# Performance work log

Measured on AMD Instinct MI355X. Metric: run time of the kernel, lower is better.

## Reference

```python
import jax, jax.numpy as jnp
import numpy as np

B, S, E, H = 4, 4096, 256, 2048
EPS = 1e-5

def layernorm(x, g, b):
    mu = jnp.mean(x, axis=-1, keepdims=True)
    var = jnp.mean(jnp.square(x - mu), axis=-1, keepdims=True)
    return (x - mu) * jax.lax.rsqrt(var + EPS) * g + b

def setup_inputs() -> dict:
    key = jax.random.key(0)
    ks = jax.random.split(key, 16)
    sE = 1.0 / np.sqrt(E)
    sH = 1.0 / np.sqrt(H)
    return {
        "x_embeddings": jax.random.normal(ks[0], (B, S, E), dtype=jnp.float32),
        "wq": jax.random.normal(ks[1], (E, E), dtype=jnp.float32) * sE,
        "bq": jnp.zeros((E,), jnp.float32),
        "wk": jax.random.normal(ks[2], (E, E), dtype=jnp.float32) * sE,
        "bk": jnp.zeros((E,), jnp.float32),
        "wv": jax.random.normal(ks[3], (E, E), dtype=jnp.float32) * sE,
        "bv": jnp.zeros((E,), jnp.float32),
        "w0": jax.random.normal(ks[4], (E, E), dtype=jnp.float32) * sE,
        "b0": jnp.zeros((E,), jnp.float32),
        "w1": jax.random.normal(ks[5], (E, H), dtype=jnp.float32) * sE,
        "b1": jnp.zeros((H,), jnp.float32),
        "ln_mlp_g": jnp.ones((H,), jnp.float32),
        "ln_mlp_b": jnp.zeros((H,), jnp.float32),
        "w2": jax.random.normal(ks[6], (H, E), dtype=jnp.float32) * sH,
        "b2": jnp.zeros((E,), jnp.float32),
        "ln1_g": jnp.ones((E,), jnp.float32),
        "ln1_b": jnp.zeros((E,), jnp.float32),
        "ln2_g": jnp.ones((E,), jnp.float32),
        "ln2_b": jnp.zeros((E,), jnp.float32),
    }

def reference(x_embeddings, wq, bq, wk, bk, wv, bv, w0, b0,
              w1, b1, ln_mlp_g, ln_mlp_b, w2, b2,
              ln1_g, ln1_b, ln2_g, ln2_b):
    x = x_embeddings
    q = x @ wq + bq
    k = x @ wk + bk
    v = x @ wv + bv
    # Unscaled, unmasked attention (faithful to source: no 1/sqrt(d), mask unused)
    scores = jnp.einsum('bqd,bkd->bqk', q, k)          # [B,S,S]
    probs = jax.nn.softmax(scores, axis=-1)
    attn = jnp.einsum('bqk,bkd->bqd', probs, v)        # [B,S,E]
    e = layernorm(x + attn, ln1_g, ln1_b) @ w0 + b0
    h = e @ w1 + b1                                     # [B,S,H]
    h = jax.nn.leaky_relu(layernorm(h, ln_mlp_g, ln_mlp_b))  # LnActivation: LN + LeakyReLU
    logits = h @ w2 + b2                                # [B,S,E]
    return layernorm(jax.nn.leaky_relu(logits + e), ln2_g, ln2_b)
```

## Files before the change

kernel.cpp:

```cpp
#include <hip/hip_runtime.h>

typedef unsigned short u16;
typedef unsigned int   u32;
typedef u16   u16x4 __attribute__((ext_vector_type(4)));
typedef u16   u16x8 __attribute__((ext_vector_type(8)));
typedef short s16x8 __attribute__((ext_vector_type(8)));
typedef u32   u32x4 __attribute__((ext_vector_type(4)));
typedef float f32x4 __attribute__((ext_vector_type(4)));
typedef _Float16 f16x8 __attribute__((ext_vector_type(8)));

__device__ __forceinline__ u16 f2b(float f) {
  u32 u = __builtin_bit_cast(u32, f);
  u32 r = (u + 0x7fffu + ((u >> 16) & 1u)) >> 16;
  return (u16)r;
}
__device__ __forceinline__ float b2f(u16 h) {
  return __builtin_bit_cast(float, (u32)h << 16);
}
__device__ __forceinline__ u16 f2h(float f) {
  _Float16 h = (_Float16)f;
  return __builtin_bit_cast(u16, h);
}
__device__ __forceinline__ u32 cvtpk(float a, float b) {
  u32 r; asm("v_cvt_pk_bf16_f32 %0, %1, %2" : "=v"(r) : "v"(a), "v"(b)); return r;
}

__device__ __forceinline__ void async16(void* l, const void* g) {
  __builtin_amdgcn_global_load_lds((const __attribute__((address_space(1))) u32*)g,
                                   (__attribute__((address_space(3))) u32*)l, 16, 0, 0);
}

__device__ __forceinline__ float wave_sum(float v) {
#pragma unroll
  for (int m = 32; m; m >>= 1) v += __shfl_xor(v, m, 64);
  return v;
}

constexpr int BM = 128, BN = 128, BK = 64;

template<bool SPLIT, int OMODE>
__global__ __launch_bounds__(256)
void k_gemm_bt(const u16* __restrict__ Ah, const u16* __restrict__ Al, long lda,
               const u16* __restrict__ Bh, const u16* __restrict__ Bl, long ldb,
               const float* __restrict__ bias,
               float* __restrict__ Cf, u16* __restrict__ Cb, u16* __restrict__ Cl,
               long ldc, int K)
{
  __shared__ u16 lds[(SPLIT ? 4 : 2) * BM * BK];
  const int tid = threadIdx.x;
  const long arow0 = (long)blockIdx.y * BM;
  const long bcol0 = (long)blockIdx.x * BN;

  long offA[4], offB[4];
#pragma unroll
  for (int r = 0; r < 4; ++r) {
    const int off = r * 4096 + tid * 16;
    const int row = off >> 7;
    const int colb = off & 127;
    offA[r] = (arow0 + row) * lda + (colb >> 1);
    offB[r] = (bcol0 + row) * ldb + (colb >> 1);
  }

  const int lane = tid & 63;
  const int wid = tid >> 6;
  const int wr = (wid >> 1) * 64;
  const int wc = (wid & 1) * 64;
  const int fr = lane & 15;
  const int fk = (lane >> 4) * 8;

  f32x4 acc[4][4] = {};

  for (int k0 = 0; k0 < K; k0 += BK) {
#pragma unroll
    for (int r = 0; r < 4; ++r) {
      const int loff = (r * 4096 + tid * 16) >> 1;
      async16(&lds[loff],           Ah + offA[r] + k0);
      async16(&lds[BM*BK + loff],   Bh + offB[r] + k0);
      if constexpr (SPLIT) {
        async16(&lds[2*BM*BK + loff], Al + offA[r] + k0);
        async16(&lds[3*BM*BK + loff], Bl + offB[r] + k0);
      }
    }
    __syncthreads();
#pragma unroll
    for (int kk = 0; kk < BK; kk += 32) {
      s16x8 a[4], b[4];
#pragma unroll
      for (int m = 0; m < 4; ++m)
        a[m] = *(const s16x8*)&lds[(wr + m*16 + fr) * BK + kk + fk];
#pragma unroll
      for (int n = 0; n < 4; ++n)
        b[n] = *(const s16x8*)&lds[BM*BK + (wc + n*16 + fr) * BK + kk + fk];
#pragma unroll
      for (int m = 0; m < 4; ++m)
#pragma unroll
        for (int n = 0; n < 4; ++n)
          acc[m][n] = __builtin_amdgcn_mfma_f32_16x16x32_bf16(a[m], b[n], acc[m][n], 0, 0, 0);
      if constexpr (SPLIT) {
        s16x8 al[4], bl[4];
#pragma unroll
        for (int m = 0; m < 4; ++m)
          al[m] = *(const s16x8*)&lds[2*BM*BK + (wr + m*16 + fr) * BK + kk + fk];
#pragma unroll
        for (int n = 0; n < 4; ++n)
          bl[n] = *(const s16x8*)&lds[3*BM*BK + (wc + n*16 + fr) * BK + kk + fk];
#pragma unroll
        for (int m = 0; m < 4; ++m)
#pragma unroll
          for (int n = 0; n < 4; ++n) {
            acc[m][n] = __builtin_amdgcn_mfma_f32_16x16x32_bf16(a[m], bl[n], acc[m][n], 0, 0, 0);
            acc[m][n] = __builtin_amdgcn_mfma_f32_16x16x32_bf16(al[m], b[n], acc[m][n], 0, 0, 0);
          }
      }
    }
    __syncthreads();
  }

  float bv[4];
#pragma unroll
  for (int n = 0; n < 4; ++n) {
    const long gcol = bcol0 + wc + n*16 + fr;
    bv[n] = bias ? bias[gcol] : 0.f;
  }

#pragma unroll
  for (int m = 0; m < 4; ++m) {
#pragma unroll
    for (int reg = 0; reg < 4; ++reg) {
      const long grow = arow0 + wr + m*16 + (lane >> 4) * 4 + reg;
      const long ro = grow * ldc;
#pragma unroll
      for (int n = 0; n < 4; ++n) {
        const long gcol = bcol0 + wc + n*16 + fr;
        const float val = acc[m][n][reg] + bv[n];
        if constexpr (OMODE == 0) {
          Cf[ro + gcol] = val;
        } else {
          Cb[ro + gcol] = f2b(val);
        }
      }
    }
  }
}

__global__ __launch_bounds__(256)
void k_gemm_qkv(const float* __restrict__ Af,
                const u16* __restrict__ Bh, const u16* __restrict__ Bl,
                const float* __restrict__ bias,
                u16* __restrict__ Cq, u16* __restrict__ Ck, u16* __restrict__ Cv)
{
  __shared__ float ldsA[BM * BK];
  __shared__ u16 ldsBh[BN * BK];
  __shared__ u16 ldsBl[BN * BK];
  const int tid = threadIdx.x;
  const long arow0 = (long)blockIdx.y * BM;
  const long bcol0 = (long)blockIdx.x * BN;

  long offA[8];
#pragma unroll
  for (int r = 0; r < 8; ++r) {
    const int off = r * 4096 + tid * 16;
    const int row = off >> 8;
    const int colb = off & 255;
    offA[r] = (arow0 + row) * 256 + (colb >> 2);
  }
  long offB[4];
#pragma unroll
  for (int r = 0; r < 4; ++r) {
    const int off = r * 4096 + tid * 16;
    const int row = off >> 7;
    const int colb = off & 127;
    offB[r] = (bcol0 + row) * 256 + (colb >> 1);
  }

  const int lane = tid & 63;
  const int wid = tid >> 6;
  const int wr = (wid >> 1) * 64;
  const int wc = (wid & 1) * 64;
  const int fr = lane & 15;
  const int fk = (lane >> 4) * 8;

  f32x4 acc[4][4] = {};

  for (int k0 = 0; k0 < 256; k0 += BK) {
#pragma unroll
    for (int r = 0; r < 8; ++r)
      async16((char*)ldsA + r*4096 + tid*16, Af + offA[r] + k0);
#pragma unroll
    for (int r = 0; r < 4; ++r) {
      const int loff = (r * 4096 + tid * 16) >> 1;
      async16(&ldsBh[loff], Bh + offB[r] + k0);
      async16(&ldsBl[loff], Bl + offB[r] + k0);
    }
    __syncthreads();
#pragma unroll
    for (int kk = 0; kk < BK; kk += 32) {
      s16x8 a[4], al[4];
#pragma unroll
      for (int m = 0; m < 4; ++m) {
        const float* ap = &ldsA[(wr + m*16 + fr) * BK + kk + fk];
        const float4 v0 = *(const float4*)ap;
        const float4 v1 = *(const float4*)(ap + 4);
        u32x4 H, L;
        H[0] = cvtpk(v0.x, v0.y); H[1] = cvtpk(v0.z, v0.w);
        H[2] = cvtpk(v1.x, v1.y); H[3] = cvtpk(v1.z, v1.w);
        L[0] = cvtpk(v0.x - __builtin_bit_cast(float, H[0] << 16),
                     v0.y - __builtin_bit_cast(float, H[0] & 0xffff0000u));
        L[1] = cvtpk(v0.z - __builtin_bit_cast(float, H[1] << 16),
                     v0.w - __builtin_bit_cast(float, H[1] & 0xffff0000u));
        L[2] = cvtpk(v1.x - __builtin_bit_cast(float, H[2] << 16),
                     v1.y - __builtin_bit_cast(float, H[2] & 0xffff0000u));
        L[3] = cvtpk(v1.z - __builtin_bit_cast(float, H[3] << 16),
                     v1.w - __builtin_bit_cast(float, H[3] & 0xffff0000u));
        a[m]  = __builtin_bit_cast(s16x8, H);
        al[m] = __builtin_bit_cast(s16x8, L);
      }
      s16x8 b[4], bl[4];
#pragma unroll
      for (int n = 0; n < 4; ++n) {
        b[n]  = *(const s16x8*)&ldsBh[(wc + n*16 + fr) * BK + kk + fk];
        bl[n] = *(const s16x8*)&ldsBl[(wc + n*16 + fr) * BK + kk + fk];
      }
#pragma unroll
      for (int m = 0; m < 4; ++m)
#pragma unroll
        for (int n = 0; n < 4; ++n) {
          acc[m][n] = __builtin_amdgcn_mfma_f32_16x16x32_bf16(a[m],  b[n],  acc[m][n], 0, 0, 0);
          acc[m][n] = __builtin_amdgcn_mfma_f32_16x16x32_bf16(a[m],  bl[n], acc[m][n], 0, 0, 0);
          acc[m][n] = __builtin_amdgcn_mfma_f32_16x16x32_bf16(al[m], b[n],  acc[m][n], 0, 0, 0);
        }
    }
    __syncthreads();
  }

  float bv[4];
#pragma unroll
  for (int n = 0; n < 4; ++n)
    bv[n] = bias[bcol0 + wc + n*16 + fr];

  const int band = (int)(bcol0 >> 8);
  u16* dst = (band == 0) ? Cq : (band == 1) ? Ck : Cv;

#pragma unroll
  for (int m = 0; m < 4; ++m) {
#pragma unroll
    for (int reg = 0; reg < 4; ++reg) {
      const long grow = arow0 + wr + m*16 + (lane >> 4) * 4 + reg;
#pragma unroll
      for (int n = 0; n < 4; ++n) {
        const long lc = bcol0 - (long)band*256 + wc + n*16 + fr;
        const float val = acc[m][n][reg] + bv[n];
        dst[grow * 256 + lc] = (band < 2) ? f2h(val) : f2b(val);
      }
    }
  }
}

__global__ __launch_bounds__(256)
void k_flash(const u16* __restrict__ q16, const u16* __restrict__ k16,
             const u16* __restrict__ vt,
             u16* __restrict__ attn)
{
  __shared__ u16 lkh[2][32*256];
  __shared__ float lS[32*36];
  __shared__ u16 lP[32*40];
  __shared__ float lm[32], ll[32], lsc[32];

  const int tid = threadIdx.x;
  const int lane = tid & 63, wid = tid >> 6;
  const long bo = (long)blockIdx.y * 1048576;
  const long q0 = (long)blockIdx.x * 32;

  const int fr  = lane & 15;
  const int hi2 = lane >> 4;
  const int fk  = hi2 * 8;
  const int qh_sel = wid >> 1;
  const int kh_sel = wid & 1;

  f16x8 qf[8];
  {
    const u16* qp = q16 + bo + (q0 + qh_sel*16 + fr) * 256;
#pragma unroll
    for (int c = 0; c < 8; ++c)
      qf[c] = *(const f16x8*)(qp + c*32 + fk);
  }

  if (tid < 32) { lm[tid] = -1e30f; ll[tid] = 0.f; }
  f32x4 acc[2][4] = {};

  const char* kp = (const char*)(k16 + bo);
  const u16* vbase = vt + bo;

  auto STAGE = [&](int k0s, int b) {
#pragma unroll
    for (int r = 0; r < 4; ++r) {
      const int L = r*4096 + tid*16;
      const int row = L >> 9;
      const int colb = L & 511;
      const long gb = (long)(k0s + row)*512 + (colb ^ ((row & 7) << 4));
      async16((char*)lkh[b] + L, kp + gb);
    }
  };

  STAGE(0, 0);
  __syncthreads();

  int cur = 0;
  for (int k0 = 0; k0 < 4096; k0 += 32) {
    s16x8 vb[4];
#pragma unroll
    for (int j = 0; j < 4; ++j)
      vb[j] = *(const s16x8*)(vbase + (long)(wid*64 + j*16 + fr)*4096 + k0 + fk);

    if (k0 + 32 < 4096) STAGE(k0 + 32, cur ^ 1);

    f32x4 sa = {}, sb = {};
    const int kc = kh_sel*16 + fr;
    const int swz = (kc & 7) << 4;
#pragma unroll
    for (int c = 0; c < 4; ++c) {
      const int o0 = ((2*c)*64 + hi2*16) ^ swz;
      const int o1 = ((2*c + 1)*64 + hi2*16) ^ swz;
      const f16x8 b0 = *(const f16x8*)((const char*)lkh[cur] + kc*512 + o0);
      const f16x8 b1 = *(const f16x8*)((const char*)lkh[cur] + kc*512 + o1);
      sa = __builtin_amdgcn_mfma_f32_16x16x32_f16(qf[2*c],     b0, sa, 0, 0, 0);
      sb = __builtin_amdgcn_mfma_f32_16x16x32_f16(qf[2*c + 1], b1, sb, 0, 0, 0);
    }
    const f32x4 s0 = sa + sb;
#pragma unroll
    for (int r = 0; r < 4; ++r)
      lS[(qh_sel*16 + hi2*4 + r)*36 + kh_sel*16 + fr] = s0[r];
    __syncthreads();

    {
      const int sr = tid >> 3;
      const int sc = (tid & 7) * 4;
      const float4 sv = *(const float4*)&lS[sr*36 + sc];
      float tmx = fmaxf(fmaxf(sv.x, sv.y), fmaxf(sv.z, sv.w));
#pragma unroll
      for (int m = 1; m < 8; m <<= 1) tmx = fmaxf(tmx, __shfl_xor(tmx, m, 64));
      const float mold = lm[sr];
      const float mnew = fmaxf(mold, tmx);
      const float p0 = __expf(sv.x - mnew), p1 = __expf(sv.y - mnew);
      const float p2 = __expf(sv.z - mnew), p3 = __expf(sv.w - mnew);
      float ps = p0 + p1 + p2 + p3;
#pragma unroll
      for (int m = 1; m < 8; m <<= 1) ps += __shfl_xor(ps, m, 64);
      const float scale = __expf(mold - mnew);
      if ((tid & 7) == 0) {
        lm[sr] = mnew;
        ll[sr] = ll[sr] * scale + ps;
        lsc[sr] = scale;
      }
      u16x4 pb; pb[0]=f2b(p0); pb[1]=f2b(p1); pb[2]=f2b(p2); pb[3]=f2b(p3);
      *(u16x4*)&lP[sr*40 + sc] = pb;
    }
    __syncthreads();

#pragma unroll
    for (int qm = 0; qm < 2; ++qm)
#pragma unroll
      for (int r = 0; r < 4; ++r) {
        const float s = lsc[qm*16 + hi2*4 + r];
#pragma unroll
        for (int j = 0; j < 4; ++j) acc[qm][j][r] *= s;
      }
#pragma unroll
    for (int qm = 0; qm < 2; ++qm) {
      const s16x8 pa = *(const s16x8*)&lP[(qm*16 + fr)*40 + fk];
#pragma unroll
      for (int j = 0; j < 4; ++j)
        acc[qm][j] = __builtin_amdgcn_mfma_f32_16x16x32_bf16(pa, vb[j], acc[qm][j], 0, 0, 0);
    }
    cur ^= 1;
  }

  __syncthreads();
#pragma unroll
  for (int qm = 0; qm < 2; ++qm)
#pragma unroll
    for (int r = 0; r < 4; ++r) {
      const int row = qm*16 + hi2*4 + r;
      const float inv = 1.0f / ll[row];
      u16* op = attn + bo + (q0 + row)*256 + wid*64 + fr;
#pragma unroll
      for (int j = 0; j < 4; ++j)
        op[j*16] = f2b(acc[qm][j][r] * inv);
    }
}


__global__ __launch_bounds__(256)
void k_transpose_qkv0(const float* __restrict__ wq, const float* __restrict__ wk,
                      const float* __restrict__ wv, const float* __restrict__ w0,
                      u16* __restrict__ catT_h, u16* __restrict__ catT_l,
                      u16* __restrict__ w0T,
                      const float* __restrict__ bq, const float* __restrict__ bk,
                      const float* __restrict__ bv, float* __restrict__ catBias) {
  __shared__ float t[32][33];
  const int z = blockIdx.z;
  const float* in = (z == 0) ? wq : (z == 1) ? wk : (z == 2) ? wv : w0;
  const int c0 = blockIdx.x * 32, r0 = blockIdx.y * 32;
  const int tx = threadIdx.x, ty = threadIdx.y;
#pragma unroll
  for (int i = 0; i < 4; ++i)
    t[ty + i*8][tx] = in[(long)(r0 + ty + i*8) * 256 + c0 + tx];
  __syncthreads();
#pragma unroll
  for (int i = 0; i < 4; ++i) {
    const float f = t[tx][ty + i*8];
    const u16 hb = f2b(f);
    if (z < 3) {
      const long o = (long)(z*256 + c0 + ty + i*8) * 256 + r0 + tx;
      catT_h[o] = hb;
      catT_l[o] = f2b(f - b2f(hb));
    } else {
      w0T[(long)(c0 + ty + i*8) * 256 + r0 + tx] = hb;
    }
  }
  if (z == 3 && blockIdx.x == 0 && blockIdx.y == 0) {
    const int t0 = ty * 32 + tx;
    catBias[t0] = bq[t0];
    catBias[256 + t0] = bk[t0];
    catBias[512 + t0] = bv[t0];
  }
}

__global__ __launch_bounds__(256)
void k_transpose_f32ns(const float* __restrict__ in, u16* __restrict__ hi, int R, int C) {
  __shared__ float t[32][33];
  const int c0 = blockIdx.x * 32, r0 = blockIdx.y * 32;
  const int tx = threadIdx.x, ty = threadIdx.y;
#pragma unroll
  for (int i = 0; i < 4; ++i)
    t[ty + i*8][tx] = in[(long)(r0 + ty + i*8) * C + c0 + tx];
  __syncthreads();
#pragma unroll
  for (int i = 0; i < 4; ++i)
    hi[(long)(c0 + ty + i*8) * R + r0 + tx] = f2b(t[tx][ty + i*8]);
}

__global__ __launch_bounds__(256)
void k_transpose_bf16(const u16* __restrict__ in, u16* __restrict__ out,
                      int R, int C, long sIn, long sOut) {
  __shared__ u16 t[32][34];
  const int z = blockIdx.z;
  const u16* ib = in + (long)z * sIn;
  u16* ob = out + (long)z * sOut;
  const int c0 = blockIdx.x * 32, r0 = blockIdx.y * 32;
  const int tx = threadIdx.x, ty = threadIdx.y;
#pragma unroll
  for (int i = 0; i < 4; ++i)
    t[ty + i*8][tx] = ib[(long)(r0 + ty + i*8) * C + c0 + tx];
  __syncthreads();
#pragma unroll
  for (int i = 0; i < 4; ++i)
    ob[(long)(c0 + ty + i*8) * R + r0 + tx] = t[tx][ty + i*8];
}

__global__ __launch_bounds__(256)
void k_add_ln(const float* __restrict__ x, const u16* __restrict__ a,
              const float* __restrict__ g, const float* __restrict__ b,
              u16* __restrict__ out) {
  const long row = (long)blockIdx.x * 4 + (threadIdx.x >> 6);
  const int lane = threadIdx.x & 63;
  const long base = row * 256 + lane * 4;
  const float4 xv = *(const float4*)(x + base);
  const u16x4 av = *(const u16x4*)(a + base);
  float t[4] = {xv.x + b2f(av[0]), xv.y + b2f(av[1]), xv.z + b2f(av[2]), xv.w + b2f(av[3])};
  float s = t[0] + t[1] + t[2] + t[3];
  float q = t[0]*t[0] + t[1]*t[1] + t[2]*t[2] + t[3]*t[3];
  s = wave_sum(s); q = wave_sum(q);
  const float mu = s * (1.f / 256.f);
  const float var = q * (1.f / 256.f) - mu * mu;
  const float rs = rsqrtf(var + 1e-5f);
  const float4 gv = *(const float4*)(g + lane * 4);
  const float4 bv = *(const float4*)(b + lane * 4);
  u16x4 o;
  o[0] = f2b((t[0] - mu) * rs * gv.x + bv.x);
  o[1] = f2b((t[1] - mu) * rs * gv.y + bv.y);
  o[2] = f2b((t[2] - mu) * rs * gv.z + bv.z);
  o[3] = f2b((t[3] - mu) * rs * gv.w + bv.w);
  *(u16x4*)(out + base) = o;
}

__global__ __launch_bounds__(256)
void k_ln_leaky(const u16* __restrict__ h, const float* __restrict__ g,
                const float* __restrict__ b, u16* __restrict__ out) {
  const long row = blockIdx.x;
  const int tid = threadIdx.x;
  const int lane = tid & 63, wid = tid >> 6;
  const u16x8 hv = *(const u16x8*)(h + row * 2048 + tid * 8);
  float f[8];
  float s = 0.f, q = 0.f;
#pragma unroll
  for (int j = 0; j < 8; ++j) { f[j] = b2f(hv[j]); s += f[j]; q += f[j] * f[j]; }
  s = wave_sum(s); q = wave_sum(q);
  __shared__ float rs_[4], rq_[4];
  if (lane == 0) { rs_[wid] = s; rq_[wid] = q; }
  __syncthreads();
  s = rs_[0] + rs_[1] + rs_[2] + rs_[3];
  q = rq_[0] + rq_[1] + rq_[2] + rq_[3];
  const float mu = s * (1.f / 2048.f);
  const float var = q * (1.f / 2048.f) - mu * mu;
  const float rsq = rsqrtf(var + 1e-5f);
  const float4 g0 = *(const float4*)(g + tid * 8);
  const float4 g1 = *(const float4*)(g + tid * 8 + 4);
  const float4 b0 = *(const float4*)(b + tid * 8);
  const float4 b1 = *(const float4*)(b + tid * 8 + 4);
  const float gg[8] = {g0.x, g0.y, g0.z, g0.w, g1.x, g1.y, g1.z, g1.w};
  const float bb[8] = {b0.x, b0.y, b0.z, b0.w, b1.x, b1.y, b1.z, b1.w};
  u16x8 o;
#pragma unroll
  for (int j = 0; j < 8; ++j) {
    float y = (f[j] - mu) * rsq * gg[j] + bb[j];
    y = y > 0.f ? y : 0.01f * y;
    o[j] = f2b(y);
  }
  *(u16x8*)(out + row * 2048 + tid * 8) = o;
}

__global__ __launch_bounds__(256)
void k_final(const float* __restrict__ lg, const u16* __restrict__ e,
             const float* __restrict__ g, const float* __restrict__ b,
             float* __restrict__ out) {
  const long row = (long)blockIdx.x * 4 + (threadIdx.x >> 6);
  const int lane = threadIdx.x & 63;
  const long base = row * 256 + lane * 4;
  const float4 lv = *(const float4*)(lg + base);
  const u16x4 ev = *(const u16x4*)(e + base);
  float t[4] = {lv.x + b2f(ev[0]), lv.y + b2f(ev[1]), lv.z + b2f(ev[2]), lv.w + b2f(ev[3])};
#pragma unroll
  for (int j = 0; j < 4; ++j) t[j] = t[j] > 0.f ? t[j] : 0.01f * t[j];
  float s = t[0] + t[1] + t[2] + t[3];
  float q = t[0]*t[0] + t[1]*t[1] + t[2]*t[2] + t[3]*t[3];
  s = wave_sum(s); q = wave_sum(q);
  const float mu = s * (1.f / 256.f);
  const float var = q * (1.f / 256.f) - mu * mu;
  const float rs = rsqrtf(var + 1e-5f);
  const float4 gv = *(const float4*)(g + lane * 4);
  const float4 bv = *(const float4*)(b + lane * 4);
  float4 o;
  o.x = (t[0] - mu) * rs * gv.x + bv.x;
  o.y = (t[1] - mu) * rs * gv.y + bv.y;
  o.z = (t[2] - mu) * rs * gv.z + bv.z;
  o.w = (t[3] - mu) * rs * gv.w + bv.w;
  *(float4*)(out + base) = o;
}


extern "C" void kernel_launch(void* const* d_in, const int* in_sizes, int n_in,
                              void* d_out, int out_size, void* d_ws, size_t ws_size,
                              hipStream_t stream) {
  const float* x   = (const float*)d_in[0];
  const float* wq  = (const float*)d_in[1];
  const float* bq  = (const float*)d_in[2];
  const float* wk  = (const float*)d_in[3];
  const float* bk  = (const float*)d_in[4];
  const float* wv  = (const float*)d_in[5];
  const float* bv_ = (const float*)d_in[6];
  const float* w0  = (const float*)d_in[7];
  const float* b0  = (const float*)d_in[8];
  const float* w1  = (const float*)d_in[9];
  const float* b1  = (const float*)d_in[10];
  const float* lmg = (const float*)d_in[11];
  const float* lmb = (const float*)d_in[12];
  const float* w2  = (const float*)d_in[13];
  const float* b2  = (const float*)d_in[14];
  const float* l1g = (const float*)d_in[15];
  const float* l1b = (const float*)d_in[16];
  const float* l2g = (const float*)d_in[17];
  const float* l2b = (const float*)d_in[18];

  char* ws = (char*)d_ws;
  float* out = (float*)d_out;

  u16* q16    = (u16*)(ws + 0);
  u16* k16    = (u16*)(ws + 16777216);
  u16* vT     = (u16*)(ws + 33554432);
  u16* v_b    = (u16*)(ws + 58720256);
  u16* attn_b = (u16*)(ws + 67108864);
  u16* ln1    = (u16*)(ws + 75497472);
  u16* e_b    = (u16*)(ws + 83886080);
  float* logits = (float*)(ws + 92274688);
  u16* h_b    = (u16*)(ws + 0);
  u16* catT_h = (u16*)(ws + 109051904);
  u16* catT_l = (u16*)(ws + 109445120);
  u16* w0T    = (u16*)(ws + 109838336);
  u16* w1T    = (u16*)(ws + 109969408);
  u16* w2T    = (u16*)(ws + 111017984);
  float* catBias = (float*)(ws + 112066560);

  const dim3 t256(256);
  const dim3 tr(32, 8);

  k_transpose_qkv0<<<dim3(8, 8, 4), tr, 0, stream>>>(
      wq, wk, wv, w0, catT_h, catT_l, w0T, bq, bk, bv_, catBias);
  k_transpose_f32ns<<<dim3(64, 8), tr, 0, stream>>>(w1, w1T, 256, 2048);
  k_transpose_f32ns<<<dim3(8, 64), tr, 0, stream>>>(w2, w2T, 2048, 256);

  k_gemm_qkv<<<dim3(6, 128), t256, 0, stream>>>(
      x, catT_h, catT_l, catBias, q16, k16, v_b);
  k_transpose_bf16<<<dim3(8, 128, 4), tr, 0, stream>>>(v_b, vT, 4096, 256, 1048576, 1048576);

  k_flash<<<dim3(128, 4), t256, 0, stream>>>(q16, k16, vT, attn_b);

  k_add_ln<<<4096, t256, 0, stream>>>(x, attn_b, l1g, l1b, ln1);

  k_gemm_bt<false, 1><<<dim3(2, 128), t256, 0, stream>>>(
      ln1, nullptr, 256, w0T, nullptr, 256, b0, nullptr, e_b, nullptr, 256, 256);
  k_gemm_bt<false, 1><<<dim3(16, 128), t256, 0, stream>>>(
      e_b, nullptr, 256, w1T, nullptr, 256, b1, nullptr, h_b, nullptr, 2048, 256);
  k_ln_leaky<<<16384, t256, 0, stream>>>(h_b, lmg, lmb, h_b);
  k_gemm_bt<false, 0><<<dim3(2, 128), t256, 0, stream>>>(
      h_b, nullptr, 2048, w2T, nullptr, 2048, b2, logits, nullptr, nullptr, 256, 2048);
  k_final<<<4096, t256, 0, stream>>>(logits, e_b, l2g, l2b, out);
}
```

Baseline: 364.6 us.

## Widen flash attention key tile to 64 and fuse residual-add layernorm epilogue

The flash attention kernel now processes 64 keys per iteration instead of 32. This halves the number of barrier-separated softmax rounds and doubles the K staging buffer in shared memory. The separate add+layernorm kernel is removed; its work moves into the flash epilogue, which adds x and reduces row statistics across waves through shared memory. This saves one launch and one bf16 round trip of the attention output, at the cost of more LDS and registers per block, which may lower occupancy.

After: 334.0 us, median of 2. -8.4%, faster.

```diff
diff --git a/kernel.cpp b/kernel.cpp
--- a/kernel.cpp
+++ b/kernel.cpp
@@ -259,11 +259,13 @@
 __global__ __launch_bounds__(256)
 void k_flash(const u16* __restrict__ q16, const u16* __restrict__ k16,
              const u16* __restrict__ vt,
-             u16* __restrict__ attn)
+             const float* __restrict__ x,
+             const float* __restrict__ g, const float* __restrict__ b,
+             u16* __restrict__ ln1)
 {
-  __shared__ u16 lkh[2][32*256];
-  __shared__ float lS[32*36];
-  __shared__ u16 lP[32*40];
+  __shared__ u16 lkh[2][64*256];
+  __shared__ float lS[32*68];
+  __shared__ u16 lP[32*72];
   __shared__ float lm[32], ll[32], lsc[32];
 
   const int tid = threadIdx.x;
@@ -291,14 +293,14 @@
   const char* kp = (const char*)(k16 + bo);
   const u16* vbase = vt + bo;
 
-  auto STAGE = [&](int k0s, int b) {
-#pragma unroll
-    for (int r = 0; r < 4; ++r) {
+  auto STAGE = [&](int k0s, int bsel) {
+#pragma unroll
+    for (int r = 0; r < 8; ++r) {
       const int L = r*4096 + tid*16;
       const int row = L >> 9;
       const int colb = L & 511;
       const long gb = (long)(k0s + row)*512 + (colb ^ ((row & 7) << 4));
-      async16((char*)lkh[b] + L, kp + gb);
+      async16((char*)lkh[bsel] + L, kp + gb);
     }
   };
 
@@ -306,44 +308,51 @@
   __syncthreads();
 
   int cur = 0;
-  for (int k0 = 0; k0 < 4096; k0 += 32) {
-    s16x8 vb[4];
-#pragma unroll
-    for (int j = 0; j < 4; ++j)
-      vb[j] = *(const s16x8*)(vbase + (long)(wid*64 + j*16 + fr)*4096 + k0 + fk);
-
-    if (k0 + 32 < 4096) STAGE(k0 + 32, cur ^ 1);
-
-    f32x4 sa = {}, sb = {};
-    const int kc = kh_sel*16 + fr;
-    const int swz = (kc & 7) << 4;
-#pragma unroll
-    for (int c = 0; c < 4; ++c) {
-      const int o0 = ((2*c)*64 + hi2*16) ^ swz;
-      const int o1 = ((2*c + 1)*64 + hi2*16) ^ swz;
-      const f16x8 b0 = *(const f16x8*)((const char*)lkh[cur] + kc*512 + o0);
-      const f16x8 b1 = *(const f16x8*)((const char*)lkh[cur] + kc*512 + o1);
-      sa = __builtin_amdgcn_mfma_f32_16x16x32_f16(qf[2*c],     b0, sa, 0, 0, 0);
-      sb = __builtin_amdgcn_mfma_f32_16x16x32_f16(qf[2*c + 1], b1, sb, 0, 0, 0);
-    }
-    const f32x4 s0 = sa + sb;
-#pragma unroll
-    for (int r = 0; r < 4; ++r)
-      lS[(qh_sel*16 + hi2*4 + r)*36 + kh_sel*16 + fr] = s0[r];
+  for (int k0 = 0; k0 < 4096; k0 += 64) {
+    s16x8 vb[2][4];
+#pragma unroll
+    for (int ks = 0; ks < 2; ++ks)
+#pragma unroll
+      for (int j = 0; j < 4; ++j)
+        vb[ks][j] = *(const s16x8*)(vbase + (long)(wid*64 + j*16 + fr)*4096 + k0 + ks*32 + fk);
+
+    if (k0 + 64 < 4096) STAGE(k0 + 64, cur ^ 1);
+
+    f32x4 s0 = {}, s1 = {};
+    const int kc0 = kh_sel*32 + fr;
+    const int swz = (kc0 & 7) << 4;
+#pragma unroll
+    for (int c = 0; c < 8; ++c) {
+      const int o = (c*64 + hi2*16) ^ swz;
+      const f16x8 b0 = *(const f16x8*)((const char*)lkh[cur] + kc0*512 + o);
+      const f16x8 b1 = *(const f16x8*)((const char*)lkh[cur] + (kc0 + 16)*512 + o);
+      s0 = __builtin_amdgcn_mfma_f32_16x16x32_f16(qf[c], b0, s0, 0, 0, 0);
+      s1 = __builtin_amdgcn_mfma_f32_16x16x32_f16(qf[c], b1, s1, 0, 0, 0);
+    }
+#pragma unroll
+    for (int r = 0; r < 4; ++r) {
+      const int srow = (qh_sel*16 + hi2*4 + r) * 68;
+      lS[srow + kh_sel*32 + fr]      = s0[r];
+      lS[srow + kh_sel*32 + 16 + fr] = s1[r];
+    }
     __syncthreads();
 
     {
       const int sr = tid >> 3;
-      const int sc = (tid & 7) * 4;
-      const float4 sv = *(const float4*)&lS[sr*36 + sc];
-      float tmx = fmaxf(fmaxf(sv.x, sv.y), fmaxf(sv.z, sv.w));
+      const int sc = (tid & 7) * 8;
+      const float4 sv0 = *(const float4*)&lS[sr*68 + sc];
+      const float4 sv1 = *(const float4*)&lS[sr*68 + sc + 4];
+      float tmx = fmaxf(fmaxf(fmaxf(sv0.x, sv0.y), fmaxf(sv0.z, sv0.w)),
+                        fmaxf(fmaxf(sv1.x, sv1.y), fmaxf(sv1.z, sv1.w)));
 #pragma unroll
       for (int m = 1; m < 8; m <<= 1) tmx = fmaxf(tmx, __shfl_xor(tmx, m, 64));
       const float mold = lm[sr];
       const float mnew = fmaxf(mold, tmx);
-      const float p0 = __expf(sv.x - mnew), p1 = __expf(sv.y - mnew);
-      const float p2 = __expf(sv.z - mnew), p3 = __expf(sv.w - mnew);
-      float ps = p0 + p1 + p2 + p3;
+      const float p0 = __expf(sv0.x - mnew), p1 = __expf(sv0.y - mnew);
+      const float p2 = __expf(sv0.z - mnew), p3 = __expf(sv0.w - mnew);
+      const float p4 = __expf(sv1.x - mnew), p5 = __expf(sv1.y - mnew);
+      const float p6 = __expf(sv1.z - mnew), p7 = __expf(sv1.w - mnew);
+      float ps = ((p0 + p1) + (p2 + p3)) + ((p4 + p5) + (p6 + p7));
 #pragma unroll
       for (int m = 1; m < 8; m <<= 1) ps += __shfl_xor(ps, m, 64);
       const float scale = __expf(mold - mnew);
@@ -352,8 +361,10 @@
         ll[sr] = ll[sr] * scale + ps;
         lsc[sr] = scale;
       }
-      u16x4 pb; pb[0]=f2b(p0); pb[1]=f2b(p1); pb[2]=f2b(p2); pb[3]=f2b(p3);
-      *(u16x4*)&lP[sr*40 + sc] = pb;
+      u16x8 pb;
+      pb[0]=f2b(p0); pb[1]=f2b(p1); pb[2]=f2b(p2); pb[3]=f2b(p3);
+      pb[4]=f2b(p4); pb[5]=f2b(p5); pb[6]=f2b(p6); pb[7]=f2b(p7);
+      *(u16x8*)&lP[sr*72 + sc] = pb;
     }
     __syncthreads();
 
@@ -366,26 +377,61 @@
         for (int j = 0; j < 4; ++j) acc[qm][j][r] *= s;
       }
 #pragma unroll
-    for (int qm = 0; qm < 2; ++qm) {
-      const s16x8 pa = *(const s16x8*)&lP[(qm*16 + fr)*40 + fk];
-#pragma unroll
-      for (int j = 0; j < 4; ++j)
-        acc[qm][j] = __builtin_amdgcn_mfma_f32_16x16x32_bf16(pa, vb[j], acc[qm][j], 0, 0, 0);
-    }
+    for (int qm = 0; qm < 2; ++qm)
+#pragma unroll
+      for (int ks = 0; ks < 2; ++ks) {
+        const s16x8 pa = *(const s16x8*)&lP[(qm*16 + fr)*72 + ks*32 + fk];
+#pragma unroll
+        for (int j = 0; j < 4; ++j)
+          acc[qm][j] = __builtin_amdgcn_mfma_f32_16x16x32_bf16(pa, vb[ks][j], acc[qm][j], 0, 0, 0);
+      }
     cur ^= 1;
   }
 
   __syncthreads();
+  float gv4[4], bv4[4];
+#pragma unroll
+  for (int j = 0; j < 4; ++j) {
+    gv4[j] = g[wid*64 + j*16 + fr];
+    bv4[j] = b[wid*64 + j*16 + fr];
+  }
+  const float* xb = x + bo + q0*256;
 #pragma unroll
   for (int qm = 0; qm < 2; ++qm)
 #pragma unroll
     for (int r = 0; r < 4; ++r) {
       const int row = qm*16 + hi2*4 + r;
       const float inv = 1.0f / ll[row];
-      u16* op = attn + bo + (q0 + row)*256 + wid*64 + fr;
+      const float* xp = xb + (long)row*256 + wid*64 + fr;
+      float s = 0.f, qq = 0.f;
+#pragma unroll
+      for (int j = 0; j < 4; ++j) {
+        const float t = acc[qm][j][r] * inv + xp[j*16];
+        acc[qm][j][r] = t;
+        s += t; qq += t*t;
+      }
+#pragma unroll
+      for (int m = 1; m < 16; m <<= 1) {
+        s  += __shfl_xor(s, m, 64);
+        qq += __shfl_xor(qq, m, 64);
+      }
+      if (fr == 0) { lS[row*4 + wid] = s; lS[128 + row*4 + wid] = qq; }
+    }
+  __syncthreads();
+#pragma unroll
+  for (int qm = 0; qm < 2; ++qm)
+#pragma unroll
+    for (int r = 0; r < 4; ++r) {
+      const int row = qm*16 + hi2*4 + r;
+      const float s  = (lS[row*4+0] + lS[row*4+1]) + (lS[row*4+2] + lS[row*4+3]);
+      const float qq = (lS[128+row*4+0] + lS[128+row*4+1]) + (lS[128+row*4+2] + lS[128+row*4+3]);
+      const float mu = s * (1.f / 256.f);
+      const float var = qq * (1.f / 256.f) - mu * mu;
+      const float rs = rsqrtf(var + 1e-5f);
+      u16* op = ln1 + bo + (q0 + row)*256 + wid*64 + fr;
 #pragma unroll
       for (int j = 0; j < 4; ++j)
-        op[j*16] = f2b(acc[qm][j][r] * inv);
+        op[j*16] = f2b((acc[qm][j][r] - mu) * rs * gv4[j] + bv4[j]);
     }
 }
 
@@ -456,32 +502,6 @@
 #pragma unroll
   for (int i = 0; i < 4; ++i)
     ob[(long)(c0 + ty + i*8) * R + r0 + tx] = t[tx][ty + i*8];
-}
-
-__global__ __launch_bounds__(256)
-void k_add_ln(const float* __restrict__ x, const u16* __restrict__ a,
-              const float* __restrict__ g, const float* __restrict__ b,
-              u16* __restrict__ out) {
-  const long row = (long)blockIdx.x * 4 + (threadIdx.x >> 6);
-  const int lane = threadIdx.x & 63;
-  const long base = row * 256 + lane * 4;
-  const float4 xv = *(const float4*)(x + base);
-  const u16x4 av = *(const u16x4*)(a + base);
-  float t[4] = {xv.x + b2f(av[0]), xv.y + b2f(av[1]), xv.z + b2f(av[2]), xv.w + b2f(av[3])};
-  float s = t[0] + t[1] + t[2] + t[3];
-  float q = t[0]*t[0] + t[1]*t[1] + t[2]*t[2] + t[3]*t[3];
-  s = wave_sum(s); q = wave_sum(q);
-  const float mu = s * (1.f / 256.f);
-  const float var = q * (1.f / 256.f) - mu * mu;
-  const float rs = rsqrtf(var + 1e-5f);
-  const float4 gv = *(const float4*)(g + lane * 4);
-  const float4 bv = *(const float4*)(b + lane * 4);
-  u16x4 o;
-  o[0] = f2b((t[0] - mu) * rs * gv.x + bv.x);
-  o[1] = f2b((t[1] - mu) * rs * gv.y + bv.y);
-  o[2] = f2b((t[2] - mu) * rs * gv.z + bv.z);
-  o[3] = f2b((t[3] - mu) * rs * gv.w + bv.w);
-  *(u16x4*)(out + base) = o;
 }
 
 __global__ __launch_bounds__(256)
@@ -579,7 +599,6 @@
   u16* k16    = (u16*)(ws + 16777216);
   u16* vT     = (u16*)(ws + 33554432);
   u16* v_b    = (u16*)(ws + 58720256);
-  u16* attn_b = (u16*)(ws + 67108864);
   u16* ln1    = (u16*)(ws + 75497472);
   u16* e_b    = (u16*)(ws + 83886080);
   float* logits = (float*)(ws + 92274688);
@@ -603,9 +622,7 @@
       x, catT_h, catT_l, catBias, q16, k16, v_b);
   k_transpose_bf16<<<dim3(8, 128, 4), tr, 0, stream>>>(v_b, vT, 4096, 256, 1048576, 1048576);
 
-  k_flash<<<dim3(128, 4), t256, 0, stream>>>(q16, k16, vT, attn_b);
-
-  k_add_ln<<<4096, t256, 0, stream>>>(x, attn_b, l1g, l1b, ln1);
+  k_flash<<<dim3(128, 4), t256, 0, stream>>>(q16, k16, vT, x, l1g, l1b, ln1);
 
   k_gemm_bt<false, 1><<<dim3(2, 128), t256, 0, stream>>>(
       ln1, nullptr, 256, w0T, nullptr, 256, b0, nullptr, e_b, nullptr, 256, 256);
```
